# Optimization experiments

Measured on AMD Instinct MI355X. Metric: run time of the kernel, lower is better.

The kernel has to match this reference:

```python
import jax, jax.numpy as jnp
import numpy as np

B, D_IN, H, OUT = 4096, 2048, 4096, 1000
TEMPERATURE = 0.5


def _l2_normalize(w):
    return w / jnp.linalg.norm(w, axis=1, keepdims=True)


def setup_inputs() -> dict:
    key = jax.random.key(0)
    ks = jax.random.split(key, 8)
    x = jax.random.normal(ks[0], (B, D_IN), dtype=jnp.float32)
    kohonen_weights = _l2_normalize(jax.random.normal(ks[1], (H, D_IN), dtype=jnp.float32))
    # MLP: 4096 -> 2048 -> 1024 -> 1000 (hidden_layers=2, div=2)
    def lin(k, fan_in, fan_out):
        kw, kb = jax.random.split(k)
        bound = 1.0 / np.sqrt(fan_in)
        W = jax.random.uniform(kw, (fan_out, fan_in), minval=-bound, maxval=bound, dtype=jnp.float32)
        b = jax.random.uniform(kb, (fan_out,), minval=-bound, maxval=bound, dtype=jnp.float32)
        return W, b
    w1, b1 = lin(ks[2], H, H // 2)
    w2, b2 = lin(ks[3], H // 2, H // 4)
    w3, b3 = lin(ks[4], H // 4, OUT)
    return {"x": x, "kohonen_weights": kohonen_weights,
            "w1": w1, "b1": b1, "w2": w2, "b2": b2, "w3": w3, "b3": b3}


def reference(x, kohonen_weights, w1, b1, w2, b2, w3, b3):
    # pairwise euclidean distances [B, H] via expanded GEMM (cdist p=2)
    x2 = jnp.sum(x * x, axis=1, keepdims=True)            # [B,1]
    w2sq = jnp.sum(kohonen_weights * kohonen_weights, axis=1)  # [H]
    d2 = x2 + w2sq[None, :] - 2.0 * (x @ kohonen_weights.T)
    distances = jnp.sqrt(jnp.maximum(d2, 1e-12))
    winners = jnp.argmin(distances, axis=1)
    soft = jax.nn.softmax(-distances / TEMPERATURE, axis=1)
    # MLP (dropout=0 / eval mode)
    h = jax.nn.relu(soft @ w1.T + b1)
    h = jax.nn.relu(h @ w2.T + b2)
    output = h @ w3.T + b3
    return output, winners
```

## Files before the change

### kernel.cpp

```cpp
#include <hip/hip_runtime.h>
#include <hip/hip_bf16.h>
#include <stdint.h>

typedef __attribute__((ext_vector_type(4))) float f32x4;
typedef __attribute__((ext_vector_type(8))) __bf16 bf16x8;
typedef unsigned short u16;
typedef unsigned long long u64;

__device__ __forceinline__ u16 f2bf(float f){
  unsigned u = __float_as_uint(f);
  u += 0x7fffu + ((u >> 16) & 1u);
  return (u16)(u >> 16);
}
__device__ __forceinline__ float bf2f(u16 v){
  return __uint_as_float(((unsigned)v) << 16);
}

__device__ __forceinline__ void gload16(const u16* g, u16* l){
  __builtin_amdgcn_global_load_lds(
      (__attribute__((address_space(1))) void*)g,
      (__attribute__((address_space(3))) void*)l, 16, 0, 0);
}

template<int N> __device__ __forceinline__ void waitcnt_vm(){
  if constexpr (N==0)  asm volatile("s_waitcnt vmcnt(0)" ::: "memory");
  else if constexpr (N==4)  asm volatile("s_waitcnt vmcnt(4)" ::: "memory");
  else if constexpr (N==8)  asm volatile("s_waitcnt vmcnt(8)" ::: "memory");
}

__global__ __launch_bounds__(64)
void cvt_rows2(const float* __restrict__ x, const float* __restrict__ Wk,
               u16* __restrict__ xb, u16* __restrict__ wb,
               float* __restrict__ x2, float* __restrict__ w2s)
{
#pragma clang fp contract(off)
  const int bid = blockIdx.x;
  const int row = bid & 4095;
  const float* src = (bid < 4096) ? x : Wk;
  u16* dst = (bid < 4096) ? xb : wb;
  float* sq = (bid < 4096) ? x2 : w2s;
  const int l = threadIdx.x;
  const float* r = src + (size_t)row * 2048;
  const f32x4* r4 = (const f32x4*)r;
  ushort4* d4 = (ushort4*)(dst + (size_t)row * 2048);
#pragma unroll
  for (int i = 0; i < 8; i++){
    f32x4 v = r4[l + 64*i];
    ushort4 o;
    o.x = f2bf(v.x); o.y = f2bf(v.y); o.z = f2bf(v.z); o.w = f2bf(v.w);
    d4[l + 64*i] = o;
  }
  float leaf = 0.f;
  if (l < 16){
    const f32x4* p4 = (const f32x4*)(r + l*128);
    f32x4 a0 = {0.f,0.f,0.f,0.f}, a1 = {0.f,0.f,0.f,0.f};
#pragma unroll
    for (int i = 0; i < 32; i += 2){
      f32x4 v0 = p4[i], v1 = p4[i+1];
      a0 = a0 + v0*v0;
      a1 = a1 + v1*v1;
    }
    leaf = ((a0.x+a0.y)+(a0.z+a0.w))+((a1.x+a1.y)+(a1.z+a1.w));
  }
#pragma unroll
  for (int s = 1; s < 16; s <<= 1){
    float o = __shfl_down(leaf, s);
    if ((l & (2*s - 1)) == 0) leaf = leaf + o;
  }
  if (l == 0) sq[row] = leaf;
}

__global__ __launch_bounds__(256)
void cvt_w(const float* __restrict__ w1, const float* __restrict__ w2,
           const float* __restrict__ w3,
           u16* __restrict__ w1b, u16* __restrict__ w2b, u16* __restrict__ w3b)
{
  const int N1 = 2097152;
  const int N2 = N1 + 524288;
  const int N3 = N2 + 262144;
  for (int i = blockIdx.x*256 + threadIdx.x; i < N3; i += gridDim.x*256){
    f32x4 v;
    ushort4* dp;
    if (i < N1){
      v = ((const f32x4*)w1)[i];
      dp = (ushort4*)w1b + i;
    } else if (i < N2){
      v = ((const f32x4*)w2)[i - N1];
      dp = (ushort4*)w2b + (i - N1);
    } else {
      const int j = i - N2;
      const int row = j >> 8;
      const int col4 = (j & 255)*4;
      if (row < 1000) v = *(const f32x4*)(w3 + (size_t)row*1024 + col4);
      else            v = f32x4{0.f,0.f,0.f,0.f};
      dp = (ushort4*)w3b + j;
    }
    ushort4 o;
    o.x = f2bf(v.x); o.y = f2bf(v.y); o.z = f2bf(v.z); o.w = f2bf(v.w);
    *dp = o;
  }
}

__global__ __launch_bounds__(512, 1)
void gemmN(const u16* __restrict__ A, int lda,
           const u16* __restrict__ Bm, int ldb,
           u16* __restrict__ Cb, int N, int Kpp, int nbn, int blkpp)
{
  extern __shared__ char lds[];
  const int t = threadIdx.x;
  const int nwg = gridDim.x;
  const int cpx = nwg >> 3;
  const int bid = blockIdx.x;
  const int wg  = (bid & 7)*cpx + (bid >> 3);
  const int piece = wg / blkpp;
  const int rem = wg % blkpp;
  const int bm = rem / nbn, bn = rem % nbn;
  const int brow = bm*256, bcol = bn*256;
  const u16* Ab = A + (size_t)brow*lda + (size_t)piece*Kpp;
  const u16* Bb = Bm + (size_t)bcol*ldb + (size_t)piece*Kpp;
  u16* Cp = Cb + (size_t)piece * 4096 * N;

  const int l = t & 63, w = t >> 6;
  const int wm = w >> 2, wn = w & 3;
  const int wr = wm*128, wc = wn*64;
  const int fr = l & 15, fq = l >> 4;
  const int cb0 = (fq ^ (fr & 7)) << 4;
  const int cb1 = ((4 + fq) ^ (fr & 7)) << 4;
  const int scol8 = ((t & 7) ^ ((t >> 3) & 7)) * 8;
  const int srow = t >> 3;

  const int nt = Kpp >> 6;
  f32x4 acc[8][4] = {};

  auto stageA = [&](int kt, int buf){
    const u16* s0 = Ab + (size_t)srow*lda + kt*64 + scol8;
    char* d = lds + buf*32768 + t*16;
#pragma unroll
    for (int r = 0; r < 4; r++)
      gload16(s0 + (size_t)r*64*lda, (u16*)(d + r*8192));
  };
  auto stageB = [&](int kt){
    const u16* s0 = Bb + (size_t)srow*ldb + kt*64 + scol8;
    char* d = lds + 98304 + (kt & 1)*32768 + t*16;
#pragma unroll
    for (int r = 0; r < 4; r++)
      gload16(s0 + (size_t)r*64*ldb, (u16*)(d + r*8192));
  };
  auto ldA = [&](int buf, int m, int cb)->bf16x8 {
    return *(const bf16x8*)(lds + buf*32768 + (wr + m*16 + fr)*128 + cb);
  };
  auto ldB = [&](int kt, int n, int cb)->bf16x8 {
    return *(const bf16x8*)(lds + 98304 + (kt & 1)*32768 + (wc + n*16 + fr)*128 + cb);
  };

  stageA(0, 0); stageB(0);
  __builtin_amdgcn_sched_barrier(0);
  stageA(1, 1);
  waitcnt_vm<4>();
  __builtin_amdgcn_s_barrier();

  int ra = 0, sa = 2;
  for (int kt = 0; kt < nt; kt++){
    bf16x8 av0[8], av1[8], bv0[4], bv1[4];

#pragma unroll
    for (int m = 0; m < 8; m++) av0[m] = ldA(ra, m, cb0);
#pragma unroll
    for (int n = 0; n < 4; n++) bv0[n] = ldB(kt, n, cb0);
    if (kt + 1 < nt) stageB(kt + 1);
    __builtin_amdgcn_sched_barrier(0);
    __builtin_amdgcn_s_setprio(1);
#pragma unroll
    for (int m = 0; m < 8; m++)
#pragma unroll
      for (int n = 0; n < 4; n++)
        acc[m][n] = __builtin_amdgcn_mfma_f32_16x16x32_bf16(av0[m], bv0[n], acc[m][n], 0, 0, 0);
    __builtin_amdgcn_s_setprio(0);

#pragma unroll
    for (int m = 0; m < 8; m++) av1[m] = ldA(ra, m, cb1);
#pragma unroll
    for (int n = 0; n < 4; n++) bv1[n] = ldB(kt, n, cb1);
    if (kt + 2 < nt) stageA(kt + 2, sa);
    __builtin_amdgcn_s_setprio(1);
#pragma unroll
    for (int m = 0; m < 8; m++)
#pragma unroll
      for (int n = 0; n < 4; n++)
        acc[m][n] = __builtin_amdgcn_mfma_f32_16x16x32_bf16(av1[m], bv1[n], acc[m][n], 0, 0, 0);
    __builtin_amdgcn_s_setprio(0);

    if (kt + 1 < nt){
      if (kt + 2 < nt) waitcnt_vm<4>();
      else             waitcnt_vm<0>();
      __builtin_amdgcn_s_barrier();
    }
    ra = (ra == 2) ? 0 : ra + 1;
    sa = (sa == 2) ? 0 : sa + 1;
  }

  __builtin_amdgcn_s_barrier();
  u16* ep = (u16*)(lds + w*17408);
#pragma unroll
  for (int m = 0; m < 8; m++)
#pragma unroll
    for (int n = 0; n < 4; n++)
#pragma unroll
      for (int r = 0; r < 4; r++)
        ep[(m*16 + fq*4 + r)*68 + n*16 + fr] = f2bf(acc[m][n][r]);
  asm volatile("s_waitcnt lgkmcnt(0)" ::: "memory");
  const int erow = l >> 3, ecb = (l & 7)*16;
#pragma unroll
  for (int it = 0; it < 16; it++){
    const int row = it*8 + erow;
    f32x4 v = *(const f32x4*)((const char*)ep + row*136 + ecb);
    char* gp = (char*)Cp + (((size_t)(brow + wr + row))*N + (bcol + wc))*2 + ecb;
    *(f32x4*)gp = v;
  }
}

__global__ __launch_bounds__(256)
void combine_relu(const u16* __restrict__ p0, const u16* __restrict__ p1,
                  const float* __restrict__ bias, u16* __restrict__ out)
{
  const int n4 = 4096*2048/4;
  for (int i = blockIdx.x*256 + threadIdx.x; i < n4; i += gridDim.x*256){
    ushort4 a = ((const ushort4*)p0)[i];
    ushort4 b = ((const ushort4*)p1)[i];
    const int col = (i*4) & 2047;
    f32x4 bi = *(const f32x4*)(bias + col);
    ushort4 o;
    o.x = f2bf(fmaxf(bf2f(a.x) + bf2f(b.x) + bi.x, 0.f));
    o.y = f2bf(fmaxf(bf2f(a.y) + bf2f(b.y) + bi.y, 0.f));
    o.z = f2bf(fmaxf(bf2f(a.z) + bf2f(b.z) + bi.z, 0.f));
    o.w = f2bf(fmaxf(bf2f(a.w) + bf2f(b.w) + bi.w, 0.f));
    ((ushort4*)out)[i] = o;
  }
}

template<int BM, int BN, int WM, int WN, int EPI, int MINW>
__global__ __launch_bounds__(WM*WN*64, MINW)
void gemm_p(const u16* __restrict__ A, const u16* __restrict__ Bm,
            float* __restrict__ Cf, u16* __restrict__ Cb,
            const float* __restrict__ bias,
            int M, int N, int K, int ncols, int nbn)
{
  constexpr int T  = WM*WN*64;
  constexpr int FM = BM/(WM*16);
  constexpr int FN = BN/(WN*16);
  constexpr int ABYTES = BM*64;
  constexpr int BUFB   = (BM+BN)*64;
  constexpr int RA = ABYTES/(T*16);
  constexpr int RB = (BN*64)/(T*16);
  extern __shared__ char lds[];

  const int t = threadIdx.x;
  const int nwg = gridDim.x;
  const int cpx = nwg >> 3;
  const int bid = blockIdx.x;
  const int wg  = (bid & 7)*cpx + (bid >> 3);
  const int bm = wg / nbn, bn = wg % nbn;
  const int brow = bm*BM, bcol = bn*BN;

  const int l = t & 63, w = t >> 6;
  const int wm = w / WN, wn = w % WN;
  const int wr = wm*(FM*16), wc = wn*(FN*16);
  const int fr = l & 15, fq = l >> 4, fk = fq*8;
  const int xk = fk ^ (((fr >> 1) & 3) << 3);

  const int srow = t >> 2;
  const int scol = ((t & 3)*8) ^ (((t >> 3) & 3) << 3);

  const u16* agp[RA]; const u16* bgp[RB];
#pragma unroll
  for (int r = 0; r < RA; r++)
    agp[r] = A + (size_t)(brow + r*(T>>2) + srow)*K + scol;
#pragma unroll
  for (int r = 0; r < RB; r++)
    bgp[r] = Bm + (size_t)(bcol + r*(T>>2) + srow)*K + scol;

  f32x4 acc[FM][FN] = {};
  const int nt = K >> 5;

  auto stageA = [&](int kt, int buf){
    char* dst = lds + buf*BUFB + t*16;
#pragma unroll
    for (int r = 0; r < RA; r++)
      gload16(agp[r] + (kt << 5), (u16*)(dst + r*T*16));
  };
  auto stageB = [&](int kt, int buf){
    char* dst = lds + buf*BUFB + ABYTES + t*16;
#pragma unroll
    for (int r = 0; r < RB; r++)
      gload16(bgp[r] + (kt << 5), (u16*)(dst + r*T*16));
  };

  stageA(0, 0); stageB(0, 0);
  stageA(1, 1); stageB(1, 1);
  stageA(2, 2); stageB(2, 2);
  waitcnt_vm<8>();
  __builtin_amdgcn_s_barrier();

  for (int kt = 0; kt < nt; kt++){
    const int buf = kt & 3;
    const u16* As = (const u16*)(lds + buf*BUFB);
    const u16* Bs = (const u16*)(lds + buf*BUFB + ABYTES);
    const bool pre = (kt + 3 < nt);
    const int nbuf = (kt + 3) & 3;

    bf16x8 av[FM], bv[FN];
#pragma unroll
    for (int m = 0; m < FM; m++)
      av[m] = *(const bf16x8*)(As + (wr + m*16 + fr)*32 + xk);
#pragma unroll
    for (int n = 0; n < FN; n++)
      bv[n] = *(const bf16x8*)(Bs + (wc + n*16 + fr)*32 + xk);
    if (pre){ stageA(kt + 3, nbuf); stageB(kt + 3, nbuf); }
    __builtin_amdgcn_s_setprio(1);
#pragma unroll
    for (int m = 0; m < FM; m++)
#pragma unroll
      for (int n = 0; n < FN; n++)
        acc[m][n] = __builtin_amdgcn_mfma_f32_16x16x32_bf16(av[m], bv[n], acc[m][n], 0, 0, 0);
    __builtin_amdgcn_s_setprio(0);

    if (kt + 1 < nt){
      if (kt + 3 < nt)      waitcnt_vm<8>();
      else if (kt + 2 < nt) waitcnt_vm<4>();
      else                  waitcnt_vm<0>();
      __builtin_amdgcn_s_barrier();
    }
  }

  __builtin_amdgcn_s_barrier();
  if (EPI == 1){
    u16* ep = (u16*)(lds + w*8192);
#pragma unroll
    for (int n = 0; n < FN; n++){
      const float bvv = bias[bcol + wc + n*16 + fr];
#pragma unroll
      for (int m = 0; m < FM; m++)
#pragma unroll
        for (int r = 0; r < 4; r++)
          ep[(m*16 + fq*4 + r)*64 + n*16 + fr] = f2bf(fmaxf(acc[m][n][r] + bvv, 0.f));
    }
    asm volatile("s_waitcnt lgkmcnt(0)" ::: "memory");
    const int erow = l >> 3, ecb = (l & 7)*16;
#pragma unroll
    for (int it = 0; it < 8; it++){
      const int row = it*8 + erow;
      f32x4 v = *(const f32x4*)((const char*)ep + row*128 + ecb);
      char* gp = (char*)Cb + (((size_t)(brow + wr + row))*N + (bcol + wc))*2 + ecb;
      *(f32x4*)gp = v;
    }
  } else {
    float* ep = (float*)(lds + w*16384);
#pragma unroll
    for (int n = 0; n < FN; n++){
      const int gcol = bcol + wc + n*16 + fr;
      const float bvv = (gcol < ncols) ? bias[gcol] : 0.f;
#pragma unroll
      for (int m = 0; m < FM; m++)
#pragma unroll
        for (int r = 0; r < 4; r++)
          ep[(m*16 + fq*4 + r)*64 + n*16 + fr] = acc[m][n][r] + bvv;
    }
    asm volatile("s_waitcnt lgkmcnt(0)" ::: "memory");
    const int erow = l >> 4, ecb = (l & 15)*16;
    const int gcol0 = bcol + wc + (l & 15)*4;
#pragma unroll
    for (int it = 0; it < 16; it++){
      const int row = it*4 + erow;
      f32x4 v = *(const f32x4*)((const char*)ep + row*256 + ecb);
      if (gcol0 < ncols)
        *(f32x4*)(Cf + (size_t)(brow + wr + row)*ncols + gcol0) = v;
    }
  }
}

__global__ __launch_bounds__(256)
void row_softmax(const u16* __restrict__ Sb, const float* __restrict__ x2,
                 const float* __restrict__ w2sq,
                 const float* __restrict__ x, const float* __restrict__ W,
                 u16* __restrict__ soft, float* __restrict__ winners)
{
  const int b = blockIdx.x, t = threadIdx.x;
  const float x2b = x2[b];
  const ushort4* S4 = (const ushort4*)(Sb + (size_t)b*4096);
  const f32x4* W24 = (const f32x4*)w2sq;
  float dv[16];
  float bd = 3.0e38f; int bc = 0;
#pragma unroll
  for (int i = 0; i < 4; i++){
    ushort4 s = S4[t + 256*i];
    f32x4 wv = W24[t + 256*i];
    float sf[4] = {bf2f(s.x), bf2f(s.y), bf2f(s.z), bf2f(s.w)};
#pragma unroll
    for (int j = 0; j < 4; j++){
      float u = x2b + wv[j];
      float d2 = u - 2.0f*sf[j];
      float d = __fsqrt_rn(fmaxf(d2, 1e-12f));
      dv[i*4 + j] = d;
      if (d < bd){ bd = d; bc = (t + 256*i)*4 + j; }
    }
  }
  u64 key = ((u64)__float_as_uint(bd) << 32) | (unsigned)bc;
#pragma unroll
  for (int s = 1; s < 64; s <<= 1){
    u64 o = __shfl_xor(key, s);
    if (o < key) key = o;
  }
  __shared__ u64 wk[4];
  __shared__ double csum[4];
  __shared__ float fred[4];
  __shared__ int ccnt;
  __shared__ int cand[32];
  if ((t & 63) == 0) wk[t >> 6] = key;
  if (t == 0) ccnt = 0;
  __syncthreads();
  u64 k0 = wk[0];
  if (wk[1] < k0) k0 = wk[1];
  if (wk[2] < k0) k0 = wk[2];
  if (wk[3] < k0) k0 = wk[3];
  const float dmin = __uint_as_float((unsigned)(k0 >> 32));

  const float thr = dmin + 0.01f;
#pragma unroll
  for (int i = 0; i < 4; i++)
#pragma unroll
    for (int j = 0; j < 4; j++)
      if (dv[i*4 + j] <= thr){
        int p = atomicAdd(&ccnt, 1);
        if (p < 32) cand[p] = (t + 256*i)*4 + j;
      }
  __syncthreads();
  const int nc = min(ccnt, 32);

  float bestd = 3.0e38f; int besti = 0x7fffffff;
  const f32x4* xp = (const f32x4*)(x + (size_t)b*2048) + t*2;
  f32x4 xv0 = xp[0], xv1 = xp[1];
  for (int c = 0; c < nc; c++){
    const int h = cand[c];
    const f32x4* wp = (const f32x4*)(W + (size_t)h*2048) + t*2;
    f32x4 wv0 = wp[0], wv1 = wp[1];
    double a = 0.0;
#pragma unroll
    for (int j = 0; j < 4; j++) a += (double)xv0[j]*(double)wv0[j];
#pragma unroll
    for (int j = 0; j < 4; j++) a += (double)xv1[j]*(double)wv1[j];
#pragma unroll
    for (int s = 1; s < 64; s <<= 1) a += __shfl_xor(a, s);
    if ((t & 63) == 0) csum[t >> 6] = a;
    __syncthreads();
    if (t == 0){
      double tt = (csum[0] + csum[1]) + (csum[2] + csum[3]);
      float t32 = (float)tt;
      float u = x2b + w2sq[h];
      float d2 = u - 2.0f*t32;
      float d = __fsqrt_rn(fmaxf(d2, 1e-12f));
      if (d < bestd || (d == bestd && h < besti)){ bestd = d; besti = h; }
    }
    __syncthreads();
  }
  if (t == 0) winners[b] = (float)besti;

  float es = 0.f;
#pragma unroll
  for (int i = 0; i < 16; i++) es += __expf(-2.0f*(dv[i] - dmin));
#pragma unroll
  for (int s = 1; s < 64; s <<= 1) es += __shfl_xor(es, s);
  if ((t & 63) == 0) fred[t >> 6] = es;
  __syncthreads();
  const float tot = (fred[0] + fred[1]) + (fred[2] + fred[3]);
  const float inv = 1.0f / tot;
  ushort4* o4 = (ushort4*)(soft + (size_t)b*4096);
#pragma unroll
  for (int i = 0; i < 4; i++){
    ushort4 o;
    o.x = f2bf(__expf(-2.0f*(dv[i*4+0] - dmin))*inv);
    o.y = f2bf(__expf(-2.0f*(dv[i*4+1] - dmin))*inv);
    o.z = f2bf(__expf(-2.0f*(dv[i*4+2] - dmin))*inv);
    o.w = f2bf(__expf(-2.0f*(dv[i*4+3] - dmin))*inv);
    o4[t + 256*i] = o;
  }
}

extern "C" void kernel_launch(void* const* d_in, const int* in_sizes, int n_in,
                              void* d_out, int out_size, void* d_ws, size_t ws_size,
                              hipStream_t stream)
{
  const float* x  = (const float*)d_in[0];
  const float* Wk = (const float*)d_in[1];
  const float* w1 = (const float*)d_in[2];
  const float* b1 = (const float*)d_in[3];
  const float* w2 = (const float*)d_in[4];
  const float* b2 = (const float*)d_in[5];
  const float* w3 = (const float*)d_in[6];
  const float* b3 = (const float*)d_in[7];
  float* out = (float*)d_out;
  float* winners = out + (size_t)4096*1000;

  char* ws = (char*)d_ws;
  const size_t MB = 1u << 20;
  u16* Sb    = (u16*)(ws);
  u16* soft  = (u16*)(ws + 32*MB);
  u16* w1b   = (u16*)(ws + 64*MB);
  u16* w2b   = (u16*)(ws + 80*MB);
  u16* w3b   = (u16*)(ws + 84*MB);
  float* x2  = (float*)(ws + 86*MB);
  float* w2s = x2 + 4096;
  u16* xb    = (u16*)(ws + 88*MB);
  u16* wb    = (u16*)(ws + 104*MB);
  u16* P0    = (u16*)(ws + 88*MB);
  u16* P1    = (u16*)(ws + 104*MB);
  u16* h1    = (u16*)(ws);
  u16* h2    = (u16*)(ws + 16*MB);

  cvt_rows2<<<8192, 64, 0, stream>>>(x, Wk, xb, wb, x2, w2s);
  cvt_w<<<2048, 256, 0, stream>>>(w1, w2, w3, w1b, w2b, w3b);

  hipFuncSetAttribute((const void*)gemmN,
                      hipFuncAttributeMaxDynamicSharedMemorySize, 163840);

  gemmN<<<256, 512, 163840, stream>>>(xb, 2048, wb, 2048, Sb,
                                      4096, 2048, 16, 256);

  row_softmax<<<4096, 256, 0, stream>>>(Sb, x2, w2s, x, Wk, soft, winners);

  gemmN<<<256, 512, 163840, stream>>>(soft, 4096, w1b, 4096, P0,
                                      2048, 2048, 8, 128);
  combine_relu<<<2048, 256, 0, stream>>>(P0, P1, b1, h1);

  hipFuncSetAttribute((const void*)gemm_p<128,128,2,2,1,3>,
                      hipFuncAttributeMaxDynamicSharedMemorySize, 4*256*64);
  gemm_p<128,128,2,2,1,3><<<256, 256, 4*256*64, stream>>>(
      h1, w2b, nullptr, h2, b2, 4096, 1024, 2048, 0, 8);

  hipFuncSetAttribute((const void*)gemm_p<128,128,2,2,2,3>,
                      hipFuncAttributeMaxDynamicSharedMemorySize, 4*256*64);
  gemm_p<128,128,2,2,2,3><<<256, 256, 4*256*64, stream>>>(
      h2, w3b, out, nullptr, b3, 4096, 1024, 1024, 1000, 8);
}
```

Measured before the change: 251.0 us.

## Restructure GEMM into ping-pong wave groups with split A/B staging

Replaces the 256x256 GEMM kernel with a variant whose K step is halved to 32 and whose LDS footprint shrinks to 96KB. The two wave halves split the global-to-LDS staging, one half loading A and the other B. They are offset in phase: one half loads fragments and runs MFMAs in the same iteration, while the other runs MFMAs on the previous iteration's fragments before loading the next ones. The goal is to overlap LDS reads with matrix math across wave groups. Launch bounds now request two blocks per CU, which caps registers and may force spills of the 128-register accumulator, while the grid still has only one block per CU.

```diff
diff --git a/kernel.cpp b/kernel.cpp
--- a/kernel.cpp
+++ b/kernel.cpp
@@ -101,8 +101,8 @@
   }
 }
 
-__global__ __launch_bounds__(512, 1)
-void gemmN(const u16* __restrict__ A, int lda,
+__global__ __launch_bounds__(512, 2)
+void gemmW(const u16* __restrict__ A, int lda,
            const u16* __restrict__ Bm, int ldb,
            u16* __restrict__ Cb, int N, int Kpp, int nbn, int blkpp)
 {
@@ -114,108 +114,122 @@
   const int wg  = (bid & 7)*cpx + (bid >> 3);
   const int piece = wg / blkpp;
   const int rem = wg % blkpp;
-  const int bm = rem / nbn, bn = rem % nbn;
-  const int brow = bm*256, bcol = bn*256;
+  const int brow = (rem / nbn)*256, bcol = (rem % nbn)*256;
   const u16* Ab = A + (size_t)brow*lda + (size_t)piece*Kpp;
   const u16* Bb = Bm + (size_t)bcol*ldb + (size_t)piece*Kpp;
   u16* Cp = Cb + (size_t)piece * 4096 * N;
 
   const int l = t & 63, w = t >> 6;
-  const int wm = w >> 2, wn = w & 3;
-  const int wr = wm*128, wc = wn*64;
+  const bool gA = (w < 4);
+  const int wr = (w & 3)*0 + ((w >> 2) ? 128 : 0) + 0;
+  const int wrow = (w >> 2)*128, wcol = (w & 3)*64;
   const int fr = l & 15, fq = l >> 4;
-  const int cb0 = (fq ^ (fr & 7)) << 4;
-  const int cb1 = ((4 + fq) ^ (fr & 7)) << 4;
-  const int scol8 = ((t & 7) ^ ((t >> 3) & 7)) * 8;
-  const int srow = t >> 3;
-
-  const int nt = Kpp >> 6;
+  const int xkb = (fq ^ ((fr >> 1) & 3)) << 4;
+  const int ts = t & 255;
+  const int scol = ((ts & 3) ^ ((ts >> 3) & 3))*8;
+  const int srow = ts >> 2;
+
+  auto stageA = [&](int kt, int buf){
+    const u16* s0 = Ab + (size_t)srow*lda + kt*32 + scol;
+    char* d = lds + buf*16384 + ts*16;
+#pragma unroll
+    for (int r = 0; r < 4; r++)
+      gload16(s0 + (size_t)r*64*lda, (u16*)(d + r*4096));
+  };
+  auto stageB = [&](int kt, int buf){
+    const u16* s0 = Bb + (size_t)srow*ldb + kt*32 + scol;
+    char* d = lds + 49152 + buf*16384 + ts*16;
+#pragma unroll
+    for (int r = 0; r < 4; r++)
+      gload16(s0 + (size_t)r*64*ldb, (u16*)(d + r*4096));
+  };
+  auto ldA = [&](int buf, int m)->bf16x8 {
+    return *(const bf16x8*)(lds + buf*16384 + (wrow + m*16 + fr)*64 + xkb);
+  };
+  auto ldB = [&](int buf, int n)->bf16x8 {
+    return *(const bf16x8*)(lds + 49152 + buf*16384 + (wcol + n*16 + fr)*64 + xkb);
+  };
+
   f32x4 acc[8][4] = {};
-
-  auto stageA = [&](int kt, int buf){
-    const u16* s0 = Ab + (size_t)srow*lda + kt*64 + scol8;
-    char* d = lds + buf*32768 + t*16;
-#pragma unroll
-    for (int r = 0; r < 4; r++)
-      gload16(s0 + (size_t)r*64*lda, (u16*)(d + r*8192));
-  };
-  auto stageB = [&](int kt){
-    const u16* s0 = Bb + (size_t)srow*ldb + kt*64 + scol8;
-    char* d = lds + 98304 + (kt & 1)*32768 + t*16;
-#pragma unroll
-    for (int r = 0; r < 4; r++)
-      gload16(s0 + (size_t)r*64*ldb, (u16*)(d + r*8192));
-  };
-  auto ldA = [&](int buf, int m, int cb)->bf16x8 {
-    return *(const bf16x8*)(lds + buf*32768 + (wr + m*16 + fr)*128 + cb);
-  };
-  auto ldB = [&](int kt, int n, int cb)->bf16x8 {
-    return *(const bf16x8*)(lds + 98304 + (kt & 1)*32768 + (wc + n*16 + fr)*128 + cb);
-  };
-
-  stageA(0, 0); stageB(0);
-  __builtin_amdgcn_sched_barrier(0);
-  stageA(1, 1);
+  bf16x8 av[8], bv[4];
+  const int nt = Kpp >> 5;
+
+  if (gA){ stageA(0, 0); stageA(1, 1); }
+  else   { stageB(0, 0); stageB(1, 1); }
   waitcnt_vm<4>();
   __builtin_amdgcn_s_barrier();
 
-  int ra = 0, sa = 2;
+  int rb = 0, sb = 2;
   for (int kt = 0; kt < nt; kt++){
-    bf16x8 av0[8], av1[8], bv0[4], bv1[4];
-
-#pragma unroll
-    for (int m = 0; m < 8; m++) av0[m] = ldA(ra, m, cb0);
-#pragma unroll
-    for (int n = 0; n < 4; n++) bv0[n] = ldB(kt, n, cb0);
-    if (kt + 1 < nt) stageB(kt + 1);
-    __builtin_amdgcn_sched_barrier(0);
-    __builtin_amdgcn_s_setprio(1);
-#pragma unroll
-    for (int m = 0; m < 8; m++)
-#pragma unroll
-      for (int n = 0; n < 4; n++)
-        acc[m][n] = __builtin_amdgcn_mfma_f32_16x16x32_bf16(av0[m], bv0[n], acc[m][n], 0, 0, 0);
-    __builtin_amdgcn_s_setprio(0);
-
-#pragma unroll
-    for (int m = 0; m < 8; m++) av1[m] = ldA(ra, m, cb1);
-#pragma unroll
-    for (int n = 0; n < 4; n++) bv1[n] = ldB(kt, n, cb1);
-    if (kt + 2 < nt) stageA(kt + 2, sa);
-    __builtin_amdgcn_s_setprio(1);
-#pragma unroll
-    for (int m = 0; m < 8; m++)
-#pragma unroll
-      for (int n = 0; n < 4; n++)
-        acc[m][n] = __builtin_amdgcn_mfma_f32_16x16x32_bf16(av1[m], bv1[n], acc[m][n], 0, 0, 0);
-    __builtin_amdgcn_s_setprio(0);
-
+    if (gA){
+#pragma unroll
+      for (int m = 0; m < 8; m++) av[m] = ldA(rb, m);
+#pragma unroll
+      for (int n = 0; n < 4; n++) bv[n] = ldB(rb, n);
+      if (kt + 2 < nt) stageA(kt + 2, sb);
+      __builtin_amdgcn_s_setprio(1);
+#pragma unroll
+      for (int m = 0; m < 8; m++)
+#pragma unroll
+        for (int n = 0; n < 4; n++)
+          acc[m][n] = __builtin_amdgcn_mfma_f32_16x16x32_bf16(av[m], bv[n], acc[m][n], 0, 0, 0);
+      __builtin_amdgcn_s_setprio(0);
+    } else {
+      if (kt > 0){
+        __builtin_amdgcn_s_setprio(1);
+#pragma unroll
+        for (int m = 0; m < 8; m++)
+#pragma unroll
+          for (int n = 0; n < 4; n++)
+            acc[m][n] = __builtin_amdgcn_mfma_f32_16x16x32_bf16(av[m], bv[n], acc[m][n], 0, 0, 0);
+        __builtin_amdgcn_s_setprio(0);
+      }
+      if (kt + 2 < nt) stageB(kt + 2, sb);
+#pragma unroll
+      for (int m = 0; m < 8; m++) av[m] = ldA(rb, m);
+#pragma unroll
+      for (int n = 0; n < 4; n++) bv[n] = ldB(rb, n);
+      asm volatile("s_waitcnt lgkmcnt(0)" ::: "memory");
+    }
     if (kt + 1 < nt){
       if (kt + 2 < nt) waitcnt_vm<4>();
       else             waitcnt_vm<0>();
       __builtin_amdgcn_s_barrier();
     }
-    ra = (ra == 2) ? 0 : ra + 1;
-    sa = (sa == 2) ? 0 : sa + 1;
+    rb = (rb + 1 == 3) ? 0 : rb + 1;
+    sb = (sb + 1 == 3) ? 0 : sb + 1;
+  }
+  if (!gA){
+    __builtin_amdgcn_s_setprio(1);
+#pragma unroll
+    for (int m = 0; m < 8; m++)
+#pragma unroll
+      for (int n = 0; n < 4; n++)
+        acc[m][n] = __builtin_amdgcn_mfma_f32_16x16x32_bf16(av[m], bv[n], acc[m][n], 0, 0, 0);
+    __builtin_amdgcn_s_setprio(0);
   }
 
   __builtin_amdgcn_s_barrier();
-  u16* ep = (u16*)(lds + w*17408);
-#pragma unroll
-  for (int m = 0; m < 8; m++)
-#pragma unroll
-    for (int n = 0; n < 4; n++)
-#pragma unroll
-      for (int r = 0; r < 4; r++)
-        ep[(m*16 + fq*4 + r)*68 + n*16 + fr] = f2bf(acc[m][n][r]);
-  asm volatile("s_waitcnt lgkmcnt(0)" ::: "memory");
+  u16* ep = (u16*)(lds + w*8704);
   const int erow = l >> 3, ecb = (l & 7)*16;
 #pragma unroll
-  for (int it = 0; it < 16; it++){
-    const int row = it*8 + erow;
-    f32x4 v = *(const f32x4*)((const char*)ep + row*136 + ecb);
-    char* gp = (char*)Cp + (((size_t)(brow + wr + row))*N + (bcol + wc))*2 + ecb;
-    *(f32x4*)gp = v;
+  for (int h = 0; h < 2; h++){
+#pragma unroll
+    for (int m = 0; m < 4; m++)
+#pragma unroll
+      for (int n = 0; n < 4; n++)
+#pragma unroll
+        for (int r = 0; r < 4; r++)
+          ep[(m*16 + fq*4 + r)*68 + n*16 + fr] = f2bf(acc[h*4 + m][n][r]);
+    asm volatile("s_waitcnt lgkmcnt(0)" ::: "memory");
+#pragma unroll
+    for (int it = 0; it < 8; it++){
+      const int row = it*8 + erow;
+      f32x4 v = *(const f32x4*)((const char*)ep + row*136 + ecb);
+      char* gp = (char*)Cp + (((size_t)(brow + wrow + h*64 + row))*N + (bcol + wcol))*2 + ecb;
+      *(f32x4*)gp = v;
+    }
+    asm volatile("s_waitcnt lgkmcnt(0)" ::: "memory");
   }
 }
 
@@ -519,16 +533,16 @@
   cvt_rows2<<<8192, 64, 0, stream>>>(x, Wk, xb, wb, x2, w2s);
   cvt_w<<<2048, 256, 0, stream>>>(w1, w2, w3, w1b, w2b, w3b);
 
-  hipFuncSetAttribute((const void*)gemmN,
-                      hipFuncAttributeMaxDynamicSharedMemorySize, 163840);
-
-  gemmN<<<256, 512, 163840, stream>>>(xb, 2048, wb, 2048, Sb,
-                                      4096, 2048, 16, 256);
+  hipFuncSetAttribute((const void*)gemmW,
+                      hipFuncAttributeMaxDynamicSharedMemorySize, 98304);
+
+  gemmW<<<256, 512, 98304, stream>>>(xb, 2048, wb, 2048, Sb,
+                                     4096, 2048, 16, 256);
 
   row_softmax<<<4096, 256, 0, stream>>>(Sb, x2, w2s, x, Wk, soft, winners);
 
-  gemmN<<<256, 512, 163840, stream>>>(soft, 4096, w1b, 4096, P0,
-                                      2048, 2048, 8, 128);
+  gemmW<<<256, 512, 98304, stream>>>(soft, 4096, w1b, 4096, P0,
+                                     2048, 2048, 8, 128);
   combine_relu<<<2048, 256, 0, stream>>>(P0, P1, b1, h1);
 
   hipFuncSetAttribute((const void*)gemm_p<128,128,2,2,1,3>,
```

Measured after the change: 259.4 us. 1.03x slower.

## Replace split-K 256x256 GEMM with 256x128 full-K kernel and fused bias-ReLU

Applied to the files above, without the earlier changes.

Swaps the 256x256-tile GEMM, which used split-K for the first MLP layer, for a 256x128-tile kernel with a K-step of 32 and a 4-deep LDS ring. The kernel walks the full K and applies bias and ReLU in its epilogue, so the combine_relu pass and the bf16 partial-sum buffers go away. This removes one kernel launch and the partial-sum round trip through memory, and it avoids rounding the partial sums to bf16 before they are added. The distance GEMM now launches 512 smaller tiles, which gives less data reuse per tile and more barriers per K. The gemm_p epilogue row stride is also padded to 68 to reduce LDS bank conflicts.

```diff
diff --git a/kernel.cpp b/kernel.cpp
--- a/kernel.cpp
+++ b/kernel.cpp
@@ -24,6 +24,7 @@
 
 template<int N> __device__ __forceinline__ void waitcnt_vm(){
   if constexpr (N==0)  asm volatile("s_waitcnt vmcnt(0)" ::: "memory");
+  else if constexpr (N==3)  asm volatile("s_waitcnt vmcnt(3)" ::: "memory");
   else if constexpr (N==4)  asm volatile("s_waitcnt vmcnt(4)" ::: "memory");
   else if constexpr (N==8)  asm volatile("s_waitcnt vmcnt(8)" ::: "memory");
 }
@@ -101,10 +102,12 @@
   }
 }
 
+template<int EPI>
 __global__ __launch_bounds__(512, 1)
-void gemmN(const u16* __restrict__ A, int lda,
+void gemmF(const u16* __restrict__ A, int lda,
            const u16* __restrict__ Bm, int ldb,
-           u16* __restrict__ Cb, int N, int Kpp, int nbn, int blkpp)
+           u16* __restrict__ Cb, const float* __restrict__ bias,
+           int N, int K, int nbn)
 {
   extern __shared__ char lds[];
   const int t = threadIdx.x;
@@ -112,129 +115,111 @@
   const int cpx = nwg >> 3;
   const int bid = blockIdx.x;
   const int wg  = (bid & 7)*cpx + (bid >> 3);
-  const int piece = wg / blkpp;
-  const int rem = wg % blkpp;
-  const int bm = rem / nbn, bn = rem % nbn;
-  const int brow = bm*256, bcol = bn*256;
-  const u16* Ab = A + (size_t)brow*lda + (size_t)piece*Kpp;
-  const u16* Bb = Bm + (size_t)bcol*ldb + (size_t)piece*Kpp;
-  u16* Cp = Cb + (size_t)piece * 4096 * N;
+  const int brow = (wg / nbn)*256, bcol = (wg % nbn)*128;
+  const u16* Ab = A + (size_t)brow*lda;
+  const u16* Bb = Bm + (size_t)bcol*ldb;
 
   const int l = t & 63, w = t >> 6;
-  const int wm = w >> 2, wn = w & 3;
-  const int wr = wm*128, wc = wn*64;
+  const int wrow = (w >> 1)*64, wcol = (w & 1)*64;
   const int fr = l & 15, fq = l >> 4;
-  const int cb0 = (fq ^ (fr & 7)) << 4;
-  const int cb1 = ((4 + fq) ^ (fr & 7)) << 4;
-  const int scol8 = ((t & 7) ^ ((t >> 3) & 7)) * 8;
-  const int srow = t >> 3;
-
-  const int nt = Kpp >> 6;
-  f32x4 acc[8][4] = {};
-
-  auto stageA = [&](int kt, int buf){
-    const u16* s0 = Ab + (size_t)srow*lda + kt*64 + scol8;
-    char* d = lds + buf*32768 + t*16;
-#pragma unroll
-    for (int r = 0; r < 4; r++)
-      gload16(s0 + (size_t)r*64*lda, (u16*)(d + r*8192));
+  const int xkb = (fq ^ ((fr >> 1) & 3)) << 4;
+  const int srow = t >> 2;
+  const int scol = ((t & 3) ^ ((t >> 3) & 3))*8;
+
+  auto stage = [&](int kt){
+    const int buf = kt & 3;
+    char* d = lds + buf*24576 + t*16;
+    const u16* sA = Ab + (size_t)srow*lda + kt*32 + scol;
+    gload16(sA, (u16*)d);
+    gload16(sA + (size_t)128*lda, (u16*)(d + 8192));
+    const u16* sB = Bb + (size_t)srow*ldb + kt*32 + scol;
+    gload16(sB, (u16*)(d + 16384));
   };
-  auto stageB = [&](int kt){
-    const u16* s0 = Bb + (size_t)srow*ldb + kt*64 + scol8;
-    char* d = lds + 98304 + (kt & 1)*32768 + t*16;
-#pragma unroll
-    for (int r = 0; r < 4; r++)
-      gload16(s0 + (size_t)r*64*ldb, (u16*)(d + r*8192));
+  auto ldA = [&](const char* base, int m)->bf16x8 {
+    return *(const bf16x8*)(base + (wrow + m*16 + fr)*64 + xkb);
   };
-  auto ldA = [&](int buf, int m, int cb)->bf16x8 {
-    return *(const bf16x8*)(lds + buf*32768 + (wr + m*16 + fr)*128 + cb);
+  auto ldB = [&](const char* base, int n)->bf16x8 {
+    return *(const bf16x8*)(base + 16384 + (wcol + n*16 + fr)*64 + xkb);
   };
-  auto ldB = [&](int kt, int n, int cb)->bf16x8 {
-    return *(const bf16x8*)(lds + 98304 + (kt & 1)*32768 + (wc + n*16 + fr)*128 + cb);
-  };
-
-  stageA(0, 0); stageB(0);
-  __builtin_amdgcn_sched_barrier(0);
-  stageA(1, 1);
-  waitcnt_vm<4>();
+
+  f32x4 acc[4][4] = {};
+  bf16x8 a0[4], b0[4], a1[4], b1[4];
+  const int nt = K >> 5;
+
+  stage(0); stage(1); stage(2);
+  waitcnt_vm<3>();
   __builtin_amdgcn_s_barrier();
-
-  int ra = 0, sa = 2;
-  for (int kt = 0; kt < nt; kt++){
-    bf16x8 av0[8], av1[8], bv0[4], bv1[4];
-
-#pragma unroll
-    for (int m = 0; m < 8; m++) av0[m] = ldA(ra, m, cb0);
-#pragma unroll
-    for (int n = 0; n < 4; n++) bv0[n] = ldB(kt, n, cb0);
-    if (kt + 1 < nt) stageB(kt + 1);
-    __builtin_amdgcn_sched_barrier(0);
-    __builtin_amdgcn_s_setprio(1);
-#pragma unroll
-    for (int m = 0; m < 8; m++)
-#pragma unroll
-      for (int n = 0; n < 4; n++)
-        acc[m][n] = __builtin_amdgcn_mfma_f32_16x16x32_bf16(av0[m], bv0[n], acc[m][n], 0, 0, 0);
-    __builtin_amdgcn_s_setprio(0);
-
-#pragma unroll
-    for (int m = 0; m < 8; m++) av1[m] = ldA(ra, m, cb1);
-#pragma unroll
-    for (int n = 0; n < 4; n++) bv1[n] = ldB(kt, n, cb1);
-    if (kt + 2 < nt) stageA(kt + 2, sa);
-    __builtin_amdgcn_s_setprio(1);
-#pragma unroll
-    for (int m = 0; m < 8; m++)
-#pragma unroll
-      for (int n = 0; n < 4; n++)
-        acc[m][n] = __builtin_amdgcn_mfma_f32_16x16x32_bf16(av1[m], bv1[n], acc[m][n], 0, 0, 0);
-    __builtin_amdgcn_s_setprio(0);
-
-    if (kt + 1 < nt){
-      if (kt + 2 < nt) waitcnt_vm<4>();
+#pragma unroll
+  for (int m = 0; m < 4; m++) a0[m] = ldA(lds, m);
+#pragma unroll
+  for (int n = 0; n < 4; n++) b0[n] = ldB(lds, n);
+
+  for (int kt = 0; kt < nt; kt += 2){
+    {
+      const char* bn = lds + ((kt + 1) & 3)*24576;
+#pragma unroll
+      for (int m = 0; m < 4; m++) a1[m] = ldA(bn, m);
+#pragma unroll
+      for (int n = 0; n < 4; n++) b1[n] = ldB(bn, n);
+      if (kt + 3 < nt) stage(kt + 3);
+      __builtin_amdgcn_s_setprio(1);
+#pragma unroll
+      for (int m = 0; m < 4; m++)
+#pragma unroll
+        for (int n = 0; n < 4; n++)
+          acc[m][n] = __builtin_amdgcn_mfma_f32_16x16x32_bf16(a0[m], b0[n], acc[m][n], 0, 0, 0);
+      __builtin_amdgcn_s_setprio(0);
+      if (kt + 3 < nt) waitcnt_vm<3>();
       else             waitcnt_vm<0>();
       __builtin_amdgcn_s_barrier();
     }
-    ra = (ra == 2) ? 0 : ra + 1;
-    sa = (sa == 2) ? 0 : sa + 1;
+    {
+      if (kt + 2 < nt){
+        const char* bn = lds + ((kt + 2) & 3)*24576;
+#pragma unroll
+        for (int m = 0; m < 4; m++) a0[m] = ldA(bn, m);
+#pragma unroll
+        for (int n = 0; n < 4; n++) b0[n] = ldB(bn, n);
+        if (kt + 4 < nt) stage(kt + 4);
+      }
+      __builtin_amdgcn_s_setprio(1);
+#pragma unroll
+      for (int m = 0; m < 4; m++)
+#pragma unroll
+        for (int n = 0; n < 4; n++)
+          acc[m][n] = __builtin_amdgcn_mfma_f32_16x16x32_bf16(a1[m], b1[n], acc[m][n], 0, 0, 0);
+      __builtin_amdgcn_s_setprio(0);
+      if (kt + 2 < nt){
+        if (kt + 4 < nt) waitcnt_vm<3>();
+        else             waitcnt_vm<0>();
+        __builtin_amdgcn_s_barrier();
+      }
+    }
   }
 
   __builtin_amdgcn_s_barrier();
-  u16* ep = (u16*)(lds + w*17408);
-#pragma unroll
-  for (int m = 0; m < 8; m++)
-#pragma unroll
-    for (int n = 0; n < 4; n++)
-#pragma unroll
-      for (int r = 0; r < 4; r++)
-        ep[(m*16 + fq*4 + r)*68 + n*16 + fr] = f2bf(acc[m][n][r]);
+  u16* ep = (u16*)(lds + w*8704);
+#pragma unroll
+  for (int n = 0; n < 4; n++){
+    float bvv = 0.f;
+    if (EPI == 1) bvv = bias[bcol + wcol + n*16 + fr];
+#pragma unroll
+    for (int m = 0; m < 4; m++)
+#pragma unroll
+      for (int r = 0; r < 4; r++){
+        float v = acc[m][n][r];
+        if (EPI == 1) v = fmaxf(v + bvv, 0.f);
+        ep[(m*16 + fq*4 + r)*68 + n*16 + fr] = f2bf(v);
+      }
+  }
   asm volatile("s_waitcnt lgkmcnt(0)" ::: "memory");
   const int erow = l >> 3, ecb = (l & 7)*16;
 #pragma unroll
-  for (int it = 0; it < 16; it++){
+  for (int it = 0; it < 8; it++){
     const int row = it*8 + erow;
     f32x4 v = *(const f32x4*)((const char*)ep + row*136 + ecb);
-    char* gp = (char*)Cp + (((size_t)(brow + wr + row))*N + (bcol + wc))*2 + ecb;
+    char* gp = (char*)Cb + (((size_t)(brow + wrow + row))*N + (bcol + wcol))*2 + ecb;
     *(f32x4*)gp = v;
-  }
-}
-
-__global__ __launch_bounds__(256)
-void combine_relu(const u16* __restrict__ p0, const u16* __restrict__ p1,
-                  const float* __restrict__ bias, u16* __restrict__ out)
-{
-  const int n4 = 4096*2048/4;
-  for (int i = blockIdx.x*256 + threadIdx.x; i < n4; i += gridDim.x*256){
-    ushort4 a = ((const ushort4*)p0)[i];
-    ushort4 b = ((const ushort4*)p1)[i];
-    const int col = (i*4) & 2047;
-    f32x4 bi = *(const f32x4*)(bias + col);
-    ushort4 o;
-    o.x = f2bf(fmaxf(bf2f(a.x) + bf2f(b.x) + bi.x, 0.f));
-    o.y = f2bf(fmaxf(bf2f(a.y) + bf2f(b.y) + bi.y, 0.f));
-    o.z = f2bf(fmaxf(bf2f(a.z) + bf2f(b.z) + bi.z, 0.f));
-    o.w = f2bf(fmaxf(bf2f(a.w) + bf2f(b.w) + bi.w, 0.f));
-    ((ushort4*)out)[i] = o;
   }
 }
 
@@ -334,7 +319,7 @@
 
   __builtin_amdgcn_s_barrier();
   if (EPI == 1){
-    u16* ep = (u16*)(lds + w*8192);
+    u16* ep = (u16*)(lds + w*8704);
 #pragma unroll
     for (int n = 0; n < FN; n++){
       const float bvv = bias[bcol + wc + n*16 + fr];
@@ -342,14 +327,14 @@
       for (int m = 0; m < FM; m++)
 #pragma unroll
         for (int r = 0; r < 4; r++)
-          ep[(m*16 + fq*4 + r)*64 + n*16 + fr] = f2bf(fmaxf(acc[m][n][r] + bvv, 0.f));
+          ep[(m*16 + fq*4 + r)*68 + n*16 + fr] = f2bf(fmaxf(acc[m][n][r] + bvv, 0.f));
     }
     asm volatile("s_waitcnt lgkmcnt(0)" ::: "memory");
     const int erow = l >> 3, ecb = (l & 7)*16;
 #pragma unroll
     for (int it = 0; it < 8; it++){
       const int row = it*8 + erow;
-      f32x4 v = *(const f32x4*)((const char*)ep + row*128 + ecb);
+      f32x4 v = *(const f32x4*)((const char*)ep + row*136 + ecb);
       char* gp = (char*)Cb + (((size_t)(brow + wr + row))*N + (bcol + wc))*2 + ecb;
       *(f32x4*)gp = v;
     }
@@ -511,25 +496,24 @@
   float* w2s = x2 + 4096;
   u16* xb    = (u16*)(ws + 88*MB);
   u16* wb    = (u16*)(ws + 104*MB);
-  u16* P0    = (u16*)(ws + 88*MB);
-  u16* P1    = (u16*)(ws + 104*MB);
   u16* h1    = (u16*)(ws);
   u16* h2    = (u16*)(ws + 16*MB);
 
   cvt_rows2<<<8192, 64, 0, stream>>>(x, Wk, xb, wb, x2, w2s);
   cvt_w<<<2048, 256, 0, stream>>>(w1, w2, w3, w1b, w2b, w3b);
 
-  hipFuncSetAttribute((const void*)gemmN,
-                      hipFuncAttributeMaxDynamicSharedMemorySize, 163840);
-
-  gemmN<<<256, 512, 163840, stream>>>(xb, 2048, wb, 2048, Sb,
-                                      4096, 2048, 16, 256);
+  hipFuncSetAttribute((const void*)gemmF<0>,
+                      hipFuncAttributeMaxDynamicSharedMemorySize, 98304);
+  hipFuncSetAttribute((const void*)gemmF<1>,
+                      hipFuncAttributeMaxDynamicSharedMemorySize, 98304);
+
+  gemmF<0><<<512, 512, 98304, stream>>>(xb, 2048, wb, 2048, Sb, nullptr,
+                                        4096, 2048, 32);
 
   row_softmax<<<4096, 256, 0, stream>>>(Sb, x2, w2s, x, Wk, soft, winners);
 
-  gemmN<<<256, 512, 163840, stream>>>(soft, 4096, w1b, 4096, P0,
-                                      2048, 2048, 8, 128);
-  combine_relu<<<2048, 256, 0, stream>>>(P0, P1, b1, h1);
+  gemmF<1><<<256, 512, 98304, stream>>>(soft, 4096, w1b, 4096, h1, b1,
+                                        2048, 4096, 16);
 
   hipFuncSetAttribute((const void*)gemm_p<128,128,2,2,1,3>,
                       hipFuncAttributeMaxDynamicSharedMemorySize, 4*256*64);
```

Measured after the change: 274.2 us, median of 3. 9.3% more time.
